# Kernel tuning notes

Hardware: AMD Instinct MI355X
Metric: run time of the kernel (lower is better)

Reference implementation:

```python
import jax, jax.numpy as jnp
import numpy as np

N_LAYERS = 5
EMB = 300
DK = 256
N_NODES = 50000
N_EDGES = 200000
B = 1000
NPER = N_NODES // B  # 50 nodes per graph (uniform -> to_dense_batch is a reshape)
PAD = 16
NUM_ATOM = 119


def setup_inputs() -> dict:
    key = jax.random.key(0)
    ks = jax.random.split(key, 24)
    f = lambda k, s: jax.random.normal(k, s, dtype=jnp.float32)
    return dict(
        x_type=jax.random.randint(ks[0], (N_NODES,), 0, NUM_ATOM, dtype=jnp.int32),
        x_feat=f(ks[1], (N_NODES, PAD)),
        edge_index=jax.random.randint(ks[2], (2, N_EDGES), 0, N_NODES, dtype=jnp.int32),
        edge_attr=jax.random.uniform(ks[3], (N_EDGES, 2), dtype=jnp.float32),
        metal_type=jax.random.randint(ks[4], (B,), 0, NUM_ATOM, dtype=jnp.int32),
        metal_feat=f(ks[5], (B, 17)),
        x_emb=f(ks[6], (NUM_ATOM, EMB)) * 0.05,
        x_weight=f(ks[7], (PAD, EMB)) * 0.05,
        ew1=f(ks[8], (N_LAYERS, 2, EMB)) * 0.05,
        mlp_w=f(ks[9], (N_LAYERS, EMB, EMB)) * 0.05,
        mlp_b=jnp.zeros((N_LAYERS, EMB), jnp.float32),
        bn_g=jnp.ones((N_LAYERS, EMB), jnp.float32),
        bn_b=jnp.zeros((N_LAYERS, EMB), jnp.float32),
        bn_rm=f(ks[10], (N_LAYERS, EMB)) * 0.1,
        bn_rv=jax.random.uniform(ks[11], (N_LAYERS, EMB), dtype=jnp.float32) + 0.5,
        me1_w=f(ks[12], (EMB, 17)) * 0.05,
        me1_b=jnp.zeros((EMB,), jnp.float32),
        me2=f(ks[13], (NUM_ATOM, EMB)) * 0.05,
        wq=f(ks[14], (DK, EMB)) * 0.05,
        wk=f(ks[15], (DK, EMB)) * 0.05,
        wv=f(ks[16], (DK, EMB)) * 0.05,
        ml_w=f(ks[17], (DK, EMB)) * 0.05,
        ml_b=jnp.zeros((DK,), jnp.float32),
        lg_w=f(ks[18], (DK, EMB)) * 0.05,
        lg_b=jnp.zeros((DK,), jnp.float32),
        ph1_w=f(ks[19], (2 * DK, DK)) * 0.05,
        ph1_b=jnp.zeros((2 * DK,), jnp.float32),
        ph2_w=f(ks[20], (1, 2 * DK)) * 0.05,
        ph2_b=jnp.zeros((1,), jnp.float32),
    )


def reference(x_type, x_feat, edge_index, edge_attr, metal_type, metal_feat,
              x_emb, x_weight, ew1, mlp_w, mlp_b, bn_g, bn_b, bn_rm, bn_rv,
              me1_w, me1_b, me2, wq, wk, wv, ml_w, ml_b, lg_w, lg_b,
              ph1_w, ph1_b, ph2_w, ph2_b):
    N = x_feat.shape[0]
    Bn = metal_feat.shape[0]
    # --- node init: atom-type embedding + feature projection ---
    h = x_emb[x_type] + x_feat @ x_weight                       # [N, 300]
    # --- metal feature: Linear(17->300) + Embedding(119,300) ---
    mf = (metal_feat @ me1_w.T + me1_b + me2[metal_type])[:, None, :]  # [B, 1, 300]
    # --- add self loops once (same every layer) ---
    loops = jnp.arange(N, dtype=edge_index.dtype)
    row = jnp.concatenate([edge_index[0], loops])               # [E+N] source
    col = jnp.concatenate([edge_index[1], loops])               # [E+N] target
    sl_attr = jnp.zeros((N, 2), edge_attr.dtype).at[:, 1].set(4.0)
    ea_full = jnp.concatenate([edge_attr, sl_attr], axis=0)     # [E+N, 2]
    eps = 1e-5
    for l in range(N_LAYERS):
        edge_fea = ea_full @ ew1[l]                             # [E+N, 300]
        # message: MLP(x_j + edge_attr), gather -> GEMM -> scatter-add
        msg = jax.nn.relu((h[row] + edge_fea) @ mlp_w[l].T + mlp_b[l])
        h = jax.ops.segment_sum(msg, col, num_segments=N)       # aggr='add'
        # BatchNorm1d (eval: running stats)
        h = (h - bn_rm[l]) * jax.lax.rsqrt(bn_rv[l] + eps) * bn_g[l] + bn_b[l]
        if l < N_LAYERS - 1:
            h = jax.nn.relu(h)  # dropout(p=0) is identity
    # --- CoordiNet, apool='none': dense batch (uniform graphs -> reshape) ---
    dense = h.reshape(Bn, -1, EMB)                              # [B, NPER, 300]
    Q = mf @ wq.T                                               # [B, 1, 256]
    K = dense @ wk.T                                            # [B, NPER, 256]
    V = dense @ wv.T
    scores = jnp.einsum('bqd,bkd->bqk', Q, K) / jnp.sqrt(jnp.asarray(DK, h.dtype))
    attention = jax.nn.softmax(scores, axis=-1) @ V             # [B, 1, 256]
    metal2 = jax.nn.relu(mf @ ml_w.T + ml_b)
    graph_fea = dense.mean(axis=1, keepdims=True)               # global_mean_pool
    lig = jax.nn.relu(graph_fea @ lg_w.T + lg_b)
    feature = jax.nn.relu(attention) + metal2 + lig             # [B, 1, 256]
    # --- pre_head: Linear -> Softplus -> Linear ---
    out = jax.nn.softplus(feature @ ph1_w.T + ph1_b) @ ph2_w.T + ph2_b  # [B, 1, 1]
    return out
```

## Files before the change

### kernel.cpp

```cpp
#include <hip/hip_runtime.h>
#include <hip/hip_bf16.h>
#include <math.h>

#define NNODES  50000
#define NEDGES  200000
#define NTOT    250000
#define EMB     300
#define LDK     320
#define MPAD    50048
#define NLAYERS 5
#define NSCAN   49
#define NPW     4

struct EdgeRec { int r; float c0, c1; };

typedef __attribute__((ext_vector_type(8))) short short8;
typedef __attribute__((ext_vector_type(4))) short short4v;
typedef __attribute__((ext_vector_type(4))) float floatx4;

__device__ inline void gll16(const void* g, void* s) {
    __builtin_amdgcn_global_load_lds((const __attribute__((address_space(1))) unsigned*)g,
                                     (__attribute__((address_space(3))) unsigned*)s, 16, 0, 0);
}

__global__ void k_trall(const float* __restrict__ wv, const float* __restrict__ lg_w,
                        const float* __restrict__ ph1_w, const float* __restrict__ me1_w,
                        float* __restrict__ wvT, float* __restrict__ lgwT,
                        float* __restrict__ ph1wT, float* __restrict__ me1wT) {
    int idx = blockIdx.x * 256 + threadIdx.x;
    if (idx < 76800) { int r = idx / 300, c = idx % 300; wvT[c * 256 + r] = wv[idx]; return; }
    idx -= 76800;
    if (idx < 76800) { int r = idx / 300, c = idx % 300; lgwT[c * 256 + r] = lg_w[idx]; return; }
    idx -= 76800;
    if (idx < 131072) { int r = idx / 256, c = idx % 256; ph1wT[c * 512 + r] = ph1_w[idx]; return; }
    idx -= 131072;
    if (idx < 5100) { int r = idx / 17, c = idx % 17; me1wT[c * 300 + r] = me1_w[idx]; }
}

__global__ void k_cvt(const float* __restrict__ w, __hip_bfloat16* __restrict__ wb) {
    int idx = blockIdx.x * 256 + threadIdx.x;
    if (idx >= 5 * 320 * 320) return;
    int l = idx / 102400, r = idx % 102400, n = r / 320, k = r % 320;
    float v = (n < 300 && k < 300) ? w[l * 90000 + n * 300 + k] : 0.f;
    wb[idx] = __float2bfloat16(v);
}

__global__ void k_cvt2(const float* __restrict__ wq, const float* __restrict__ ml_w,
                       const float* __restrict__ wk,
                       __hip_bfloat16* __restrict__ wcat, __hip_bfloat16* __restrict__ wkTb) {
    int idx = blockIdx.x * 256 + threadIdx.x;
    if (idx < 512 * 320) {
        int r = idx / 320, k = idx % 320;
        float v = 0.f;
        if (k < 300) v = (r < 256) ? wq[r * 300 + k] : ml_w[(r - 256) * 300 + k];
        wcat[idx] = __float2bfloat16(v);
        return;
    }
    idx -= 512 * 320;
    if (idx < 320 * 256) {
        int c = idx / 256, j = idx % 256;
        float v = (c < 300) ? wk[j * 300 + c] : 0.f;
        wkTb[idx] = __float2bfloat16(v);
    }
}

__global__ __launch_bounds__(256) void k_mf(const int* __restrict__ mt, const float* __restrict__ mfeat,
                                            const float* __restrict__ me1wT, const float* __restrict__ me1b,
                                            const float* __restrict__ me2,
                                            __hip_bfloat16* __restrict__ mfb) {
    int idx = blockIdx.x * 256 + threadIdx.x;
    if (idx >= 1000 * 300) return;
    int g = idx / 300, c = idx % 300;
    float v = me1b[c] + me2[(size_t)mt[g] * 300 + c];
    #pragma unroll
    for (int k = 0; k < 17; ++k) v += mfeat[g * 17 + k] * me1wT[k * 300 + c];
    mfb[(size_t)g * 320 + c] = __float2bfloat16(v);
}

__global__ __launch_bounds__(256) void k_mm(const __hip_bfloat16* __restrict__ A, int lda,
                                            const __hip_bfloat16* __restrict__ B, int ldb,
                                            int K, int mode,
                                            const float* __restrict__ mlb,
                                            __hip_bfloat16* __restrict__ qb,
                                            float* __restrict__ metal2,
                                            float* __restrict__ qkout) {
    __shared__ __hip_bfloat16 As[128 * 32];
    __shared__ __hip_bfloat16 Bs[64 * 32];
    int tid = threadIdx.x, lane = tid & 63, w = tid >> 6;
    int row0 = blockIdx.x * 128, col0 = blockIdx.y * 64;

    floatx4 acc[2][4];
    #pragma unroll
    for (int i = 0; i < 2; ++i)
        #pragma unroll
        for (int j = 0; j < 4; ++j) acc[i][j] = (floatx4){0.f, 0.f, 0.f, 0.f};

    const __hip_bfloat16* ga0 = A + (size_t)(row0 + w * 32 + (lane >> 2)) * lda + (lane & 3) * 8;
    const __hip_bfloat16* ga1 = ga0 + (size_t)16 * lda;
    const __hip_bfloat16* gb  = B + (size_t)(col0 + w * 16 + (lane >> 2)) * ldb + (lane & 3) * 8;
    __hip_bfloat16* sa0 = &As[(w * 32) * 32];
    __hip_bfloat16* sa1 = &As[(w * 32 + 16) * 32];
    __hip_bfloat16* sb  = &Bs[(w * 16) * 32];

    int m15 = lane & 15, kof = (lane >> 4) * 8;

    for (int k0 = 0; k0 < K; k0 += 32) {
        __syncthreads();
        gll16(ga0 + k0, sa0);
        gll16(ga1 + k0, sa1);
        gll16(gb  + k0, sb);
        __syncthreads();

        short8 a[2], b[4];
        a[0] = *(const short8*)&As[(w * 32 +      m15) * 32 + kof];
        a[1] = *(const short8*)&As[(w * 32 + 16 + m15) * 32 + kof];
        #pragma unroll
        for (int nt = 0; nt < 4; ++nt)
            b[nt] = *(const short8*)&Bs[(nt * 16 + m15) * 32 + kof];

        #pragma unroll
        for (int mt = 0; mt < 2; ++mt)
            #pragma unroll
            for (int nt = 0; nt < 4; ++nt)
                acc[mt][nt] = __builtin_amdgcn_mfma_f32_16x16x32_bf16(a[mt], b[nt], acc[mt][nt], 0, 0, 0);
    }

    int rbase = row0 + w * 32 + (lane >> 4) * 4;
    #pragma unroll
    for (int mt = 0; mt < 2; ++mt)
        #pragma unroll
        for (int i = 0; i < 4; ++i) {
            int gr = rbase + mt * 16 + i;
            #pragma unroll
            for (int nt = 0; nt < 4; ++nt) {
                int gc = col0 + nt * 16 + m15;
                float v = acc[mt][nt][i];
                if (mode == 0) {
                    if (gc < 256) qb[(size_t)gr * 256 + gc] = __float2bfloat16(v);
                    else if (gr < 1000) metal2[(size_t)gr * 256 + (gc - 256)] = fmaxf(v + mlb[gc - 256], 0.f);
                } else {
                    if (gc < 300 && gr < 1000) qkout[(size_t)gr * 320 + gc] = v;
                }
            }
        }
}

__global__ __launch_bounds__(256) void k_init(const int* __restrict__ xt,
                                              const float* __restrict__ xf,
                                              const float* __restrict__ xemb,
                                              const float* __restrict__ xw,
                                              __hip_bfloat16* __restrict__ h) {
    int gid = blockIdx.x * 256 + threadIdx.x;
    if (gid >= NNODES * 38) return;
    int n = gid / 38, c = (gid % 38) * 8;
    bool full = (c <= 292);
    const float* er = xemb + (size_t)xt[n] * 300 + c;
    float v[8];
    float4 e0 = *(const float4*)er;
    v[0] = e0.x; v[1] = e0.y; v[2] = e0.z; v[3] = e0.w;
    if (full) { float4 e1 = *(const float4*)(er + 4); v[4] = e1.x; v[5] = e1.y; v[6] = e1.z; v[7] = e1.w; }
    else      { v[4] = v[5] = v[6] = v[7] = 0.f; }
    float fs[16];
    const float4* xf4 = (const float4*)(xf + n * 16);
    #pragma unroll
    for (int q = 0; q < 4; ++q) {
        float4 t = xf4[q];
        fs[4 * q] = t.x; fs[4 * q + 1] = t.y; fs[4 * q + 2] = t.z; fs[4 * q + 3] = t.w;
    }
    #pragma unroll
    for (int k = 0; k < 16; ++k) {
        const float* wr = xw + k * 300 + c;
        float4 w0 = *(const float4*)wr;
        v[0] += fs[k] * w0.x; v[1] += fs[k] * w0.y; v[2] += fs[k] * w0.z; v[3] += fs[k] * w0.w;
        if (full) {
            float4 w1 = *(const float4*)(wr + 4);
            v[4] += fs[k] * w1.x; v[5] += fs[k] * w1.y; v[6] += fs[k] * w1.z; v[7] += fs[k] * w1.w;
        }
    }
    alignas(16) __hip_bfloat16 ob[8];
    #pragma unroll
    for (int i = 0; i < 8; ++i) ob[i] = __float2bfloat16(v[i]);
    __hip_bfloat16* hp = h + (size_t)n * LDK + c;
    if (full) *(short8*)hp  = *(const short8*)ob;
    else      *(short4v*)hp = *(const short4v*)ob;
}

__global__ void k_count(const int* __restrict__ ei, int* __restrict__ cnt) {
    int e = blockIdx.x * blockDim.x + threadIdx.x;
    if (e >= NTOT) return;
    int c = (e < NEDGES) ? ei[NEDGES + e] : (e - NEDGES);
    atomicAdd(&cnt[c], 1);
}

__global__ __launch_bounds__(1024) void k_scan1(const int* __restrict__ cnt, int* __restrict__ off,
                                                int* __restrict__ bsum) {
    int tid = threadIdx.x;
    int gid = blockIdx.x * 1024 + tid;
    int lane = tid & 63, wv = tid >> 6;
    int v = (gid < NNODES) ? cnt[gid] : 0;
    int x = v;
    #pragma unroll
    for (int s = 1; s < 64; s <<= 1) {
        int t = __shfl_up(x, s, 64);
        if (lane >= s) x += t;
    }
    __shared__ int wsum[16];
    if (lane == 63) wsum[wv] = x;
    __syncthreads();
    if (wv == 0) {
        int w = (lane < 16) ? wsum[lane] : 0;
        #pragma unroll
        for (int s = 1; s < 16; s <<= 1) {
            int t = __shfl_up(w, s, 64);
            if (lane >= s) w += t;
        }
        if (lane < 16) wsum[lane] = w;
    }
    __syncthreads();
    int base = (wv > 0) ? wsum[wv - 1] : 0;
    int incl = x + base;
    if (gid < NNODES) off[gid] = incl - v;
    if (tid == 1023) bsum[blockIdx.x] = incl;
}

__global__ __launch_bounds__(64) void k_scan2(int* __restrict__ bsum) {
    int lane = threadIdx.x;
    int v = (lane < NSCAN) ? bsum[lane] : 0;
    int x = v;
    #pragma unroll
    for (int s = 1; s < 64; s <<= 1) {
        int t = __shfl_up(x, s, 64);
        if (lane >= s) x += t;
    }
    if (lane < NSCAN) bsum[lane] = x - v;
}

__global__ __launch_bounds__(1024) void k_scan3(int* __restrict__ off, const int* __restrict__ bsum) {
    int gid = blockIdx.x * 1024 + threadIdx.x;
    if (gid < NNODES) off[gid] += bsum[blockIdx.x];
    if (gid == 0) off[NNODES] = NTOT;
}

__global__ void k_fill(const int* __restrict__ ei, const float* __restrict__ ea,
                       const int* __restrict__ off, int* __restrict__ cur,
                       EdgeRec* __restrict__ pack) {
    int e = blockIdx.x * blockDim.x + threadIdx.x;
    if (e >= NTOT) return;
    int r, c; float c0, c1;
    if (e < NEDGES) { r = ei[e]; c = ei[NEDGES + e]; c0 = ea[2 * e]; c1 = ea[2 * e + 1]; }
    else            { r = c = e - NEDGES; c0 = 0.f; c1 = 4.f; }
    int p = atomicAdd(&cur[c], 1);
    EdgeRec rec; rec.r = r; rec.c0 = c0; rec.c1 = c1;
    pack[off[c] + p] = rec;
}

__global__ __launch_bounds__(64) void k_prep(const float* __restrict__ mlp_w, const float* __restrict__ ew1,
                                             const float* __restrict__ mlp_b, const float* __restrict__ bn_g,
                                             const float* __restrict__ bn_b, const float* __restrict__ bn_rm,
                                             const float* __restrict__ bn_rv, float* __restrict__ prm) {
    int j = blockIdx.x, l = blockIdx.y;
    int lane = threadIdx.x;
    const float* W  = mlp_w + (size_t)l * 90000 + (size_t)j * 300;
    const float* ew = ew1 + l * 600;
    float a0 = 0.f, a1 = 0.f;
    #pragma unroll
    for (int i = 0; i < 5; ++i) {
        int k = lane + i * 64;
        if (k < 300) {
            float w = W[k];
            a0 += w * ew[k];
            a1 += w * ew[300 + k];
        }
    }
    #pragma unroll
    for (int s = 32; s > 0; s >>= 1) { a0 += __shfl_xor(a0, s, 64); a1 += __shfl_xor(a1, s, 64); }
    if (lane == 0) {
        float* p = prm + l * 1520;
        p[j] = a0;
        p[304 + j] = a1;
        p[608 + j] = mlp_b[l * 300 + j];
        float sc = bn_g[l * 300 + j] * rsqrtf(bn_rv[l * 300 + j] + 1e-5f);
        p[912 + j] = sc;
        p[1216 + j] = bn_b[l * 300 + j] - bn_rm[l * 300 + j] * sc;
    }
}

__global__ __launch_bounds__(256) void k_gemm(const __hip_bfloat16* __restrict__ A,
                                              const __hip_bfloat16* __restrict__ B,
                                              __hip_bfloat16* __restrict__ C) {
    int b = blockIdx.x;
    int rowblk = (b >> 4) * 8 + (b & 7);
    if (rowblk >= 391) return;
    int row0 = rowblk * 128;
    int col0 = ((b >> 3) & 1) * 160;

    __shared__ __hip_bfloat16 As[128 * 32];
    __shared__ __hip_bfloat16 Bs[160 * 32];
    int tid = threadIdx.x;
    int lane = tid & 63, w = tid >> 6;

    floatx4 acc[2][10];
    #pragma unroll
    for (int i = 0; i < 2; ++i)
        #pragma unroll
        for (int j = 0; j < 10; ++j) acc[i][j] = (floatx4){0.f, 0.f, 0.f, 0.f};

    const __hip_bfloat16* ga0 = A + (size_t)(row0 + w * 32 + (lane >> 2)) * LDK + (lane & 3) * 8;
    const __hip_bfloat16* ga1 = ga0 + (size_t)16 * LDK;
    __hip_bfloat16* sa0 = &As[(w * 32) * 32];
    __hip_bfloat16* sa1 = &As[(w * 32 + 16) * 32];
    int brow0 = (w < 2) ? w * 48 : 96 + (w - 2) * 32;
    int nb = (w < 2) ? 3 : 2;
    const __hip_bfloat16* gb = B + (size_t)(col0 + brow0 + (lane >> 2)) * LDK + (lane & 3) * 8;
    __hip_bfloat16* sb = &Bs[brow0 * 32];

    int m15 = lane & 15, kof = (lane >> 4) * 8;

    for (int k0 = 0; k0 < LDK; k0 += 32) {
        __syncthreads();
        gll16(ga0 + k0, sa0);
        gll16(ga1 + k0, sa1);
        for (int i = 0; i < nb; ++i)
            gll16(gb + (size_t)i * 16 * LDK + k0, sb + i * 16 * 32);
        __syncthreads();

        short8 a[2], bb[10];
        a[0] = *(const short8*)&As[(w * 32 +      m15) * 32 + kof];
        a[1] = *(const short8*)&As[(w * 32 + 16 + m15) * 32 + kof];
        #pragma unroll
        for (int nt = 0; nt < 10; ++nt)
            bb[nt] = *(const short8*)&Bs[(nt * 16 + m15) * 32 + kof];

        #pragma unroll
        for (int mt = 0; mt < 2; ++mt)
            #pragma unroll
            for (int nt = 0; nt < 10; ++nt)
                acc[mt][nt] = __builtin_amdgcn_mfma_f32_16x16x32_bf16(a[mt], bb[nt], acc[mt][nt], 0, 0, 0);
    }

    int rbase = row0 + w * 32 + (lane >> 4) * 4;
    #pragma unroll
    for (int mt = 0; mt < 2; ++mt)
        #pragma unroll
        for (int i = 0; i < 4; ++i) {
            long gr = rbase + mt * 16 + i;
            #pragma unroll
            for (int nt = 0; nt < 10; ++nt)
                C[gr * LDK + col0 + nt * 16 + m15] = __float2bfloat16(acc[mt][nt][i]);
        }
}

__global__ __launch_bounds__(256) void k_aggr(const __hip_bfloat16* __restrict__ mh,
                                              const EdgeRec* __restrict__ pack,
                                              const int* __restrict__ off, const float* __restrict__ prm,
                                              __hip_bfloat16* __restrict__ h, int do_relu) {
    int wave = threadIdx.x >> 6;
    int lane = threadIdx.x & 63;
    int n0 = (blockIdx.x * 4 + wave) * NPW;
    if (n0 >= NNODES) return;

    float u0[3][2], u1[3][2], bv[3][2], sc[3][2], sh[3][2];
    #pragma unroll
    for (int i = 0; i < 3; ++i) {
        int j = 2 * lane + 128 * i;
        #pragma unroll
        for (int t = 0; t < 2; ++t) {
            bool ok = (j + t) < 300;
            u0[i][t] = ok ? prm[j + t]        : 0.f;
            u1[i][t] = ok ? prm[304 + j + t]  : 0.f;
            bv[i][t] = ok ? prm[608 + j + t]  : 0.f;
            sc[i][t] = ok ? prm[912 + j + t]  : 0.f;
            sh[i][t] = ok ? prm[1216 + j + t] : 0.f;
        }
    }

    int nend = (n0 + NPW < NNODES) ? n0 + NPW : NNODES;
    for (int n = n0; n < nend; ++n) {
        float acc[3][2];
        #pragma unroll
        for (int i = 0; i < 3; ++i) { acc[i][0] = 0.f; acc[i][1] = 0.f; }
        int p0 = off[n], p1 = off[n + 1];
        int p = p0;
        for (; p + 1 < p1; p += 2) {
            EdgeRec e0 = pack[p], e1 = pack[p + 1];
            const __hip_bfloat16* b0 = mh + (size_t)e0.r * LDK;
            const __hip_bfloat16* b1 = mh + (size_t)e1.r * LDK;
            __hip_bfloat162 hv0[3], hv1[3];
            #pragma unroll
            for (int i = 0; i < 3; ++i) {
                int j = 2 * lane + 128 * i;
                if (j < 300) {
                    hv0[i] = *(const __hip_bfloat162*)&b0[j];
                    hv1[i] = *(const __hip_bfloat162*)&b1[j];
                }
            }
            #pragma unroll
            for (int i = 0; i < 3; ++i) {
                int j = 2 * lane + 128 * i;
                if (j < 300) {
                    acc[i][0] += fmaxf(__bfloat162float(hv0[i].x) + e0.c0 * u0[i][0] + e0.c1 * u1[i][0] + bv[i][0], 0.f);
                    acc[i][1] += fmaxf(__bfloat162float(hv0[i].y) + e0.c0 * u0[i][1] + e0.c1 * u1[i][1] + bv[i][1], 0.f);
                    acc[i][0] += fmaxf(__bfloat162float(hv1[i].x) + e1.c0 * u0[i][0] + e1.c1 * u1[i][0] + bv[i][0], 0.f);
                    acc[i][1] += fmaxf(__bfloat162float(hv1[i].y) + e1.c0 * u0[i][1] + e1.c1 * u1[i][1] + bv[i][1], 0.f);
                }
            }
        }
        if (p < p1) {
            EdgeRec e0 = pack[p];
            const __hip_bfloat16* b0 = mh + (size_t)e0.r * LDK;
            #pragma unroll
            for (int i = 0; i < 3; ++i) {
                int j = 2 * lane + 128 * i;
                if (j < 300) {
                    __hip_bfloat162 hv = *(const __hip_bfloat162*)&b0[j];
                    acc[i][0] += fmaxf(__bfloat162float(hv.x) + e0.c0 * u0[i][0] + e0.c1 * u1[i][0] + bv[i][0], 0.f);
                    acc[i][1] += fmaxf(__bfloat162float(hv.y) + e0.c0 * u0[i][1] + e0.c1 * u1[i][1] + bv[i][1], 0.f);
                }
            }
        }
        #pragma unroll
        for (int i = 0; i < 3; ++i) {
            int j = 2 * lane + 128 * i;
            if (j < 300) {
                float v0 = acc[i][0] * sc[i][0] + sh[i][0];
                float v1 = acc[i][1] * sc[i][1] + sh[i][1];
                if (do_relu) { v0 = fmaxf(v0, 0.f); v1 = fmaxf(v1, 0.f); }
                __hip_bfloat162 o;
                o.x = __float2bfloat16(v0);
                o.y = __float2bfloat16(v1);
                *(__hip_bfloat162*)&h[(size_t)n * LDK + j] = o;
            }
        }
    }
}

__global__ __launch_bounds__(320) void k_pool(const __hip_bfloat16* __restrict__ h, const float* __restrict__ qk,
                                              float* __restrict__ wpool, float* __restrict__ mean) {
    int b = blockIdx.x;
    int tid = threadIdx.x;
    int wave = tid >> 6, lane = tid & 63;
    __shared__ float qk_s[300];
    __shared__ float sc[50];
    __shared__ __hip_bfloat16 hs[50][304];
    if (tid < 300) qk_s[tid] = qk[(size_t)b * 320 + tid];
    __syncthreads();
    for (int k = wave; k < 50; k += 5) {
        const __hip_bfloat16* hp = h + (long)(b * 50 + k) * LDK;
        float partial = 0.f;
        #pragma unroll
        for (int i = 0; i < 5; ++i) {
            int j = lane + i * 64;
            if (j < 300) {
                __hip_bfloat16 hv = hp[j];
                hs[k][j] = hv;
                partial += __bfloat162float(hv) * qk_s[j];
            }
        }
        #pragma unroll
        for (int s = 32; s > 0; s >>= 1) partial += __shfl_xor(partial, s, 64);
        if (lane == 0) sc[k] = partial * (1.f / 16.f);
    }
    __syncthreads();
    if (tid == 0) {
        float mx = sc[0];
        for (int k = 1; k < 50; ++k) mx = fmaxf(mx, sc[k]);
        float s = 0.f;
        for (int k = 0; k < 50; ++k) { float e = __expf(sc[k] - mx); sc[k] = e; s += e; }
        float inv = 1.f / s;
        for (int k = 0; k < 50; ++k) sc[k] *= inv;
    }
    __syncthreads();
    if (tid < 300) {
        float aw = 0.f, am = 0.f;
        for (int k = 0; k < 50; ++k) {
            float v = __bfloat162float(hs[k][tid]);
            aw += sc[k] * v;
            am += v;
        }
        wpool[b * 300 + tid] = aw;
        mean[b * 300 + tid]  = am * (1.f / 50.f);
    }
}

__global__ __launch_bounds__(512) void k_head(const float* __restrict__ wpool, const float* __restrict__ mean,
                                              const float* __restrict__ metal2,
                                              const float* __restrict__ wvT, const float* __restrict__ lgwT,
                                              const float* __restrict__ lgb,
                                              const float* __restrict__ ph1wT, const float* __restrict__ ph1b,
                                              const float* __restrict__ ph2w, const float* __restrict__ ph2b,
                                              float* __restrict__ out) {
    int b = blockIdx.x;
    int tid = threadIdx.x;
    __shared__ float wp_s[300], mn_s[300], f_s[256], red[512];
    if (tid < 300) { wp_s[tid] = wpool[b * 300 + tid]; mn_s[tid] = mean[b * 300 + tid]; }
    __syncthreads();
    if (tid < 256) {
        float att = 0.f, lg = 0.f;
        #pragma unroll 4
        for (int k = 0; k < 300; ++k) {
            att += wp_s[k] * wvT[k * 256 + tid];
            lg  += mn_s[k] * lgwT[k * 256 + tid];
        }
        lg = fmaxf(lg + lgb[tid], 0.f);
        f_s[tid] = fmaxf(att, 0.f) + metal2[b * 256 + tid] + lg;
    }
    __syncthreads();
    float a = ph1b[tid];
    #pragma unroll 8
    for (int k = 0; k < 256; ++k) a += f_s[k] * ph1wT[k * 512 + tid];
    float sp = fmaxf(a, 0.f) + log1pf(__expf(-fabsf(a)));
    red[tid] = sp * ph2w[tid];
    __syncthreads();
    for (int s = 256; s > 0; s >>= 1) {
        if (tid < s) red[tid] += red[tid + s];
        __syncthreads();
    }
    if (tid == 0) out[b] = red[0] + ph2b[0];
}

extern "C" void kernel_launch(void* const* d_in, const int* in_sizes, int n_in,
                              void* d_out, int out_size, void* d_ws, size_t ws_size,
                              hipStream_t stream) {
    const int*   x_type   = (const int*)d_in[0];
    const float* x_feat   = (const float*)d_in[1];
    const int*   eindex   = (const int*)d_in[2];
    const float* eattr    = (const float*)d_in[3];
    const int*   mtype    = (const int*)d_in[4];
    const float* mfeat    = (const float*)d_in[5];
    const float* x_emb    = (const float*)d_in[6];
    const float* x_weight = (const float*)d_in[7];
    const float* ew1      = (const float*)d_in[8];
    const float* mlp_w    = (const float*)d_in[9];
    const float* mlp_b    = (const float*)d_in[10];
    const float* bn_g     = (const float*)d_in[11];
    const float* bn_b     = (const float*)d_in[12];
    const float* bn_rm    = (const float*)d_in[13];
    const float* bn_rv    = (const float*)d_in[14];
    const float* me1_w    = (const float*)d_in[15];
    const float* me1_b    = (const float*)d_in[16];
    const float* me2      = (const float*)d_in[17];
    const float* wq       = (const float*)d_in[18];
    const float* wk       = (const float*)d_in[19];
    const float* wv       = (const float*)d_in[20];
    const float* ml_w     = (const float*)d_in[21];
    const float* ml_b     = (const float*)d_in[22];
    const float* lg_w     = (const float*)d_in[23];
    const float* lg_b     = (const float*)d_in[24];
    const float* ph1_w    = (const float*)d_in[25];
    const float* ph1_b    = (const float*)d_in[26];
    const float* ph2_w    = (const float*)d_in[27];
    const float* ph2_b    = (const float*)d_in[28];

    char* ws = (char*)d_ws;
    size_t o = 0;
    auto alloc = [&](size_t bytes) -> void* {
        void* p = ws + o;
        o += (bytes + 255) & ~(size_t)255;
        return p;
    };
    __hip_bfloat16* h    = (__hip_bfloat16*)alloc((size_t)MPAD * LDK * 2);
    __hip_bfloat16* mh   = (__hip_bfloat16*)alloc((size_t)MPAD * LDK * 2);
    __hip_bfloat16* wb   = (__hip_bfloat16*)alloc((size_t)5 * 320 * 320 * 2);
    int*     cnt    = (int*)alloc((size_t)NNODES * 4);
    int*     offs   = (int*)alloc((size_t)(NNODES + 1) * 4);
    int*     cur    = (int*)alloc((size_t)NNODES * 4);
    int*     bsum   = (int*)alloc((size_t)64 * 4);
    EdgeRec* pack   = (EdgeRec*)alloc((size_t)NTOT * sizeof(EdgeRec));
    float*   prm    = (float*)alloc((size_t)NLAYERS * 1520 * 4);
    float*   metal2 = (float*)alloc((size_t)1000 * 256 * 4);
    float*   qk     = (float*)alloc((size_t)1024 * 320 * 4);
    float*   wpool  = (float*)alloc((size_t)1000 * 300 * 4);
    float*   meanp  = (float*)alloc((size_t)1000 * 300 * 4);
    float*   wvT    = (float*)alloc((size_t)300 * 256 * 4);
    float*   lgwT   = (float*)alloc((size_t)300 * 256 * 4);
    float*   ph1wT  = (float*)alloc((size_t)256 * 512 * 4);
    float*   me1wT  = (float*)alloc((size_t)17 * 300 * 4);
    __hip_bfloat16* mfb  = (__hip_bfloat16*)alloc((size_t)1024 * 320 * 2);
    __hip_bfloat16* wcat = (__hip_bfloat16*)alloc((size_t)512 * 320 * 2);
    __hip_bfloat16* wkTb = (__hip_bfloat16*)alloc((size_t)320 * 256 * 2);
    __hip_bfloat16* qb   = (__hip_bfloat16*)alloc((size_t)1024 * 256 * 2);
    (void)ws_size; (void)in_sizes; (void)n_in; (void)out_size;

    hipMemsetAsync(cnt, 0, (size_t)NNODES * 4, stream);
    hipMemsetAsync(cur, 0, (size_t)NNODES * 4, stream);
    hipMemsetAsync(mfb, 0, (size_t)1024 * 320 * 2, stream);

    k_cvt<<<(5 * 320 * 320 + 255) / 256, 256, 0, stream>>>(mlp_w, wb);
    k_cvt2<<<(512 * 320 + 320 * 256 + 255) / 256, 256, 0, stream>>>(wq, ml_w, wk, wcat, wkTb);
    k_trall<<<(289772 + 255) / 256, 256, 0, stream>>>(wv, lg_w, ph1_w, me1_w, wvT, lgwT, ph1wT, me1wT);
    k_init<<<(NNODES * 38 + 255) / 256, 256, 0, stream>>>(x_type, x_feat, x_emb, x_weight, h);
    k_count<<<(NTOT + 255) / 256, 256, 0, stream>>>(eindex, cnt);
    k_scan1<<<NSCAN, 1024, 0, stream>>>(cnt, offs, bsum);
    k_scan2<<<1, 64, 0, stream>>>(bsum);
    k_scan3<<<NSCAN, 1024, 0, stream>>>(offs, bsum);
    k_fill<<<(NTOT + 255) / 256, 256, 0, stream>>>(eindex, eattr, offs, cur, pack);
    {
        dim3 gp(300, NLAYERS);
        k_prep<<<gp, 64, 0, stream>>>(mlp_w, ew1, mlp_b, bn_g, bn_b, bn_rm, bn_rv, prm);
    }
    k_mf<<<(1000 * 300 + 255) / 256, 256, 0, stream>>>(mtype, mfeat, me1wT, me1_b, me2, mfb);
    {
        dim3 g1(8, 8);
        k_mm<<<g1, 256, 0, stream>>>(mfb, 320, wcat, 320, 320, 0, ml_b, qb, metal2, qk);
        dim3 g2(8, 5);
        k_mm<<<g2, 256, 0, stream>>>(qb, 256, wkTb, 256, 256, 1, ml_b, qb, metal2, qk);
    }

    for (int l = 0; l < NLAYERS; ++l) {
        k_gemm<<<784, 256, 0, stream>>>(h, wb + (size_t)l * 102400, mh);
        int aggr_grid = (NNODES + 4 * NPW - 1) / (4 * NPW);
        k_aggr<<<aggr_grid, 256, 0, stream>>>(mh, pack, offs, prm + (size_t)l * 1520, h,
                                              (l < NLAYERS - 1) ? 1 : 0);
    }

    k_pool<<<1000, 320, 0, stream>>>(h, qk, wpool, meanp);
    k_head<<<1000, 512, 0, stream>>>(wpool, meanp, metal2, wvT, lgwT, lg_b,
                                     ph1wT, ph1_b, ph2_w, ph2_b, (float*)d_out);
}
```

Measured before the change: 612.4 us.

## Move node init and prediction head onto bf16 MFMA GEMMs

The node-initialisation feature projection is recast as a small bf16 MFMA GEMM (features padded to K=32) with the atom-embedding add fused into the epilogue. The per-graph scalar head kernel, which reread the transposed fp32 weights in every block, is split into tiled bf16 MFMA GEMMs for the attention-value, ligand and first pre-head projections, plus small elementwise combine and softplus/reduce kernels. The aim is to replace scalar FMA loops and repeated weight traffic with matrix-core work. In exchange it adds extra conversion passes and intermediate buffers, lowers the head to bf16 precision, and reads unwritten pad columns of the pooled buffers, which are only safe if that workspace holds no NaN or Inf.

```diff
diff --git a/kernel.cpp b/kernel.cpp
--- a/kernel.cpp
+++ b/kernel.cpp
@@ -15,26 +15,11 @@
 struct EdgeRec { int r; float c0, c1; };
 
 typedef __attribute__((ext_vector_type(8))) short short8;
-typedef __attribute__((ext_vector_type(4))) short short4v;
 typedef __attribute__((ext_vector_type(4))) float floatx4;
 
 __device__ inline void gll16(const void* g, void* s) {
     __builtin_amdgcn_global_load_lds((const __attribute__((address_space(1))) unsigned*)g,
                                      (__attribute__((address_space(3))) unsigned*)s, 16, 0, 0);
-}
-
-__global__ void k_trall(const float* __restrict__ wv, const float* __restrict__ lg_w,
-                        const float* __restrict__ ph1_w, const float* __restrict__ me1_w,
-                        float* __restrict__ wvT, float* __restrict__ lgwT,
-                        float* __restrict__ ph1wT, float* __restrict__ me1wT) {
-    int idx = blockIdx.x * 256 + threadIdx.x;
-    if (idx < 76800) { int r = idx / 300, c = idx % 300; wvT[c * 256 + r] = wv[idx]; return; }
-    idx -= 76800;
-    if (idx < 76800) { int r = idx / 300, c = idx % 300; lgwT[c * 256 + r] = lg_w[idx]; return; }
-    idx -= 76800;
-    if (idx < 131072) { int r = idx / 256, c = idx % 256; ph1wT[c * 512 + r] = ph1_w[idx]; return; }
-    idx -= 131072;
-    if (idx < 5100) { int r = idx / 17, c = idx % 17; me1wT[c * 300 + r] = me1_w[idx]; }
 }
 
 __global__ void k_cvt(const float* __restrict__ w, __hip_bfloat16* __restrict__ wb) {
@@ -62,6 +47,36 @@
         float v = (c < 300) ? wk[j * 300 + c] : 0.f;
         wkTb[idx] = __float2bfloat16(v);
     }
+}
+
+__global__ void k_cvt3(const float* __restrict__ xf, const float* __restrict__ xw,
+                       const float* __restrict__ wv, const float* __restrict__ lg_w,
+                       const float* __restrict__ ph1_w, const float* __restrict__ me1_w,
+                       __hip_bfloat16* __restrict__ xfb, __hip_bfloat16* __restrict__ xwTb,
+                       __hip_bfloat16* __restrict__ wvB, __hip_bfloat16* __restrict__ lgwB,
+                       __hip_bfloat16* __restrict__ ph1wb, float* __restrict__ me1wT) {
+    int idx = blockIdx.x * 256 + threadIdx.x;
+    if (idx < 1601536) {
+        int n = idx >> 5, k = idx & 31;
+        xfb[idx] = __float2bfloat16((n < 50000 && k < 16) ? xf[n * 16 + k] : 0.f);
+        return;
+    }
+    idx -= 1601536;
+    if (idx < 10240) {
+        int n = idx >> 5, k = idx & 31;
+        xwTb[idx] = __float2bfloat16((n < 300 && k < 16) ? xw[k * 300 + n] : 0.f);
+        return;
+    }
+    idx -= 10240;
+    if (idx < 81920) { int r = idx / 320, k = idx % 320;
+        wvB[idx] = __float2bfloat16((k < 300) ? wv[r * 300 + k] : 0.f); return; }
+    idx -= 81920;
+    if (idx < 81920) { int r = idx / 320, k = idx % 320;
+        lgwB[idx] = __float2bfloat16((k < 300) ? lg_w[r * 300 + k] : 0.f); return; }
+    idx -= 81920;
+    if (idx < 131072) { ph1wb[idx] = __float2bfloat16(ph1_w[idx]); return; }
+    idx -= 131072;
+    if (idx < 5100) { int r = idx / 17, c = idx % 17; me1wT[c * 300 + r] = me1_w[idx]; }
 }
 
 __global__ __launch_bounds__(256) void k_mf(const int* __restrict__ mt, const float* __restrict__ mfeat,
@@ -145,44 +160,130 @@
         }
 }
 
-__global__ __launch_bounds__(256) void k_init(const int* __restrict__ xt,
-                                              const float* __restrict__ xf,
-                                              const float* __restrict__ xemb,
-                                              const float* __restrict__ xw,
-                                              __hip_bfloat16* __restrict__ h) {
-    int gid = blockIdx.x * 256 + threadIdx.x;
-    if (gid >= NNODES * 38) return;
-    int n = gid / 38, c = (gid % 38) * 8;
-    bool full = (c <= 292);
-    const float* er = xemb + (size_t)xt[n] * 300 + c;
-    float v[8];
-    float4 e0 = *(const float4*)er;
-    v[0] = e0.x; v[1] = e0.y; v[2] = e0.z; v[3] = e0.w;
-    if (full) { float4 e1 = *(const float4*)(er + 4); v[4] = e1.x; v[5] = e1.y; v[6] = e1.z; v[7] = e1.w; }
-    else      { v[4] = v[5] = v[6] = v[7] = 0.f; }
-    float fs[16];
-    const float4* xf4 = (const float4*)(xf + n * 16);
-    #pragma unroll
-    for (int q = 0; q < 4; ++q) {
-        float4 t = xf4[q];
-        fs[4 * q] = t.x; fs[4 * q + 1] = t.y; fs[4 * q + 2] = t.z; fs[4 * q + 3] = t.w;
-    }
-    #pragma unroll
-    for (int k = 0; k < 16; ++k) {
-        const float* wr = xw + k * 300 + c;
-        float4 w0 = *(const float4*)wr;
-        v[0] += fs[k] * w0.x; v[1] += fs[k] * w0.y; v[2] += fs[k] * w0.z; v[3] += fs[k] * w0.w;
-        if (full) {
-            float4 w1 = *(const float4*)(wr + 4);
-            v[4] += fs[k] * w1.x; v[5] += fs[k] * w1.y; v[6] += fs[k] * w1.z; v[7] += fs[k] * w1.w;
-        }
-    }
-    alignas(16) __hip_bfloat16 ob[8];
-    #pragma unroll
-    for (int i = 0; i < 8; ++i) ob[i] = __float2bfloat16(v[i]);
-    __hip_bfloat16* hp = h + (size_t)n * LDK + c;
-    if (full) *(short8*)hp  = *(const short8*)ob;
-    else      *(short4v*)hp = *(const short4v*)ob;
+__global__ __launch_bounds__(256) void k_mm2(const __hip_bfloat16* __restrict__ A, int lda,
+                                             const __hip_bfloat16* __restrict__ B, int ldb,
+                                             int K, float* __restrict__ C, int ldc) {
+    __shared__ __hip_bfloat16 As[128 * 32];
+    __shared__ __hip_bfloat16 Bs[64 * 32];
+    int tid = threadIdx.x, lane = tid & 63, w = tid >> 6;
+    int row0 = blockIdx.x * 128, col0 = blockIdx.y * 64;
+
+    floatx4 acc[2][4];
+    #pragma unroll
+    for (int i = 0; i < 2; ++i)
+        #pragma unroll
+        for (int j = 0; j < 4; ++j) acc[i][j] = (floatx4){0.f, 0.f, 0.f, 0.f};
+
+    const __hip_bfloat16* ga0 = A + (size_t)(row0 + w * 32 + (lane >> 2)) * lda + (lane & 3) * 8;
+    const __hip_bfloat16* ga1 = ga0 + (size_t)16 * lda;
+    const __hip_bfloat16* gb  = B + (size_t)(col0 + w * 16 + (lane >> 2)) * ldb + (lane & 3) * 8;
+    __hip_bfloat16* sa0 = &As[(w * 32) * 32];
+    __hip_bfloat16* sa1 = &As[(w * 32 + 16) * 32];
+    __hip_bfloat16* sb  = &Bs[(w * 16) * 32];
+
+    int m15 = lane & 15, kof = (lane >> 4) * 8;
+
+    for (int k0 = 0; k0 < K; k0 += 32) {
+        __syncthreads();
+        gll16(ga0 + k0, sa0);
+        gll16(ga1 + k0, sa1);
+        gll16(gb  + k0, sb);
+        __syncthreads();
+
+        short8 a[2], b[4];
+        a[0] = *(const short8*)&As[(w * 32 +      m15) * 32 + kof];
+        a[1] = *(const short8*)&As[(w * 32 + 16 + m15) * 32 + kof];
+        #pragma unroll
+        for (int nt = 0; nt < 4; ++nt)
+            b[nt] = *(const short8*)&Bs[(nt * 16 + m15) * 32 + kof];
+
+        #pragma unroll
+        for (int mt = 0; mt < 2; ++mt)
+            #pragma unroll
+            for (int nt = 0; nt < 4; ++nt)
+                acc[mt][nt] = __builtin_amdgcn_mfma_f32_16x16x32_bf16(a[mt], b[nt], acc[mt][nt], 0, 0, 0);
+    }
+
+    int rbase = row0 + w * 32 + (lane >> 4) * 4;
+    #pragma unroll
+    for (int mt = 0; mt < 2; ++mt)
+        #pragma unroll
+        for (int i = 0; i < 4; ++i) {
+            int gr = rbase + mt * 16 + i;
+            #pragma unroll
+            for (int nt = 0; nt < 4; ++nt)
+                C[(size_t)gr * ldc + col0 + nt * 16 + m15] = acc[mt][nt][i];
+        }
+}
+
+__global__ __launch_bounds__(256) void k_initg(const __hip_bfloat16* __restrict__ A,
+                                               const __hip_bfloat16* __restrict__ B,
+                                               const int* __restrict__ xt,
+                                               const float* __restrict__ xemb,
+                                               __hip_bfloat16* __restrict__ h) {
+    int b = blockIdx.x;
+    int rowblk = (b >> 4) * 8 + (b & 7);
+    if (rowblk >= 391) return;
+    int row0 = rowblk * 128;
+    int col0 = ((b >> 3) & 1) * 160;
+
+    __shared__ __hip_bfloat16 As[128 * 32];
+    __shared__ __hip_bfloat16 Bs[160 * 32];
+    int tid = threadIdx.x;
+    int lane = tid & 63, w = tid >> 6;
+
+    floatx4 acc[2][10];
+    #pragma unroll
+    for (int i = 0; i < 2; ++i)
+        #pragma unroll
+        for (int j = 0; j < 10; ++j) acc[i][j] = (floatx4){0.f, 0.f, 0.f, 0.f};
+
+    const __hip_bfloat16* ga0 = A + (size_t)(row0 + w * 32 + (lane >> 2)) * 32 + (lane & 3) * 8;
+    const __hip_bfloat16* ga1 = ga0 + (size_t)16 * 32;
+    __hip_bfloat16* sa0 = &As[(w * 32) * 32];
+    __hip_bfloat16* sa1 = &As[(w * 32 + 16) * 32];
+    int brow0 = (w < 2) ? w * 48 : 96 + (w - 2) * 32;
+    int nb = (w < 2) ? 3 : 2;
+    const __hip_bfloat16* gb = B + (size_t)(col0 + brow0 + (lane >> 2)) * 32 + (lane & 3) * 8;
+    __hip_bfloat16* sb = &Bs[brow0 * 32];
+
+    int m15 = lane & 15, kof = (lane >> 4) * 8;
+
+    gll16(ga0, sa0);
+    gll16(ga1, sa1);
+    for (int i = 0; i < nb; ++i)
+        gll16(gb + (size_t)i * 16 * 32, sb + i * 16 * 32);
+    __syncthreads();
+
+    short8 a[2], bb[10];
+    a[0] = *(const short8*)&As[(w * 32 +      m15) * 32 + kof];
+    a[1] = *(const short8*)&As[(w * 32 + 16 + m15) * 32 + kof];
+    #pragma unroll
+    for (int nt = 0; nt < 10; ++nt)
+        bb[nt] = *(const short8*)&Bs[(nt * 16 + m15) * 32 + kof];
+
+    #pragma unroll
+    for (int mt = 0; mt < 2; ++mt)
+        #pragma unroll
+        for (int nt = 0; nt < 10; ++nt)
+            acc[mt][nt] = __builtin_amdgcn_mfma_f32_16x16x32_bf16(a[mt], bb[nt], acc[mt][nt], 0, 0, 0);
+
+    int rbase = row0 + w * 32 + (lane >> 4) * 4;
+    #pragma unroll
+    for (int mt = 0; mt < 2; ++mt)
+        #pragma unroll
+        for (int i = 0; i < 4; ++i) {
+            int gr = rbase + mt * 16 + i;
+            if (gr < NNODES) {
+                const float* er = xemb + (size_t)xt[gr] * 300;
+                #pragma unroll
+                for (int nt = 0; nt < 10; ++nt) {
+                    int gc = col0 + nt * 16 + m15;
+                    if (gc < 300)
+                        h[(size_t)gr * LDK + gc] = __float2bfloat16(acc[mt][nt][i] + er[gc]);
+                }
+            }
+        }
 }
 
 __global__ void k_count(const int* __restrict__ ei, int* __restrict__ cnt) {
@@ -435,7 +536,7 @@
 }
 
 __global__ __launch_bounds__(320) void k_pool(const __hip_bfloat16* __restrict__ h, const float* __restrict__ qk,
-                                              float* __restrict__ wpool, float* __restrict__ mean) {
+                                              __hip_bfloat16* __restrict__ wpb, __hip_bfloat16* __restrict__ mnb) {
     int b = blockIdx.x;
     int tid = threadIdx.x;
     int wave = tid >> 6, lane = tid & 63;
@@ -477,45 +578,40 @@
             aw += sc[k] * v;
             am += v;
         }
-        wpool[b * 300 + tid] = aw;
-        mean[b * 300 + tid]  = am * (1.f / 50.f);
-    }
-}
-
-__global__ __launch_bounds__(512) void k_head(const float* __restrict__ wpool, const float* __restrict__ mean,
-                                              const float* __restrict__ metal2,
-                                              const float* __restrict__ wvT, const float* __restrict__ lgwT,
-                                              const float* __restrict__ lgb,
-                                              const float* __restrict__ ph1wT, const float* __restrict__ ph1b,
-                                              const float* __restrict__ ph2w, const float* __restrict__ ph2b,
-                                              float* __restrict__ out) {
-    int b = blockIdx.x;
-    int tid = threadIdx.x;
-    __shared__ float wp_s[300], mn_s[300], f_s[256], red[512];
-    if (tid < 300) { wp_s[tid] = wpool[b * 300 + tid]; mn_s[tid] = mean[b * 300 + tid]; }
+        wpb[(size_t)b * 320 + tid] = __float2bfloat16(aw);
+        mnb[(size_t)b * 320 + tid] = __float2bfloat16(am * (1.f / 50.f));
+    }
+}
+
+__global__ void k_comb(const float* __restrict__ attb, const float* __restrict__ ligb,
+                       const float* __restrict__ metal2, const float* __restrict__ lg_bias,
+                       __hip_bfloat16* __restrict__ fb) {
+    int idx = blockIdx.x * 256 + threadIdx.x;
+    if (idx >= 1000 * 256) return;
+    int c = idx & 255;
+    float f = fmaxf(attb[idx], 0.f) + metal2[idx] + fmaxf(ligb[idx] + lg_bias[c], 0.f);
+    fb[idx] = __float2bfloat16(f);
+}
+
+__global__ __launch_bounds__(512) void k_out(const float* __restrict__ a2, const float* __restrict__ ph1b,
+                                             const float* __restrict__ ph2w, const float* __restrict__ ph2b,
+                                             float* __restrict__ out) {
+    int b = blockIdx.x, t = threadIdx.x;
+    int lane = t & 63, wv = t >> 6;
+    float a = a2[(size_t)b * 512 + t] + ph1b[t];
+    float sp = fmaxf(a, 0.f) + log1pf(__expf(-fabsf(a)));
+    float r = sp * ph2w[t];
+    #pragma unroll
+    for (int s = 32; s > 0; s >>= 1) r += __shfl_xor(r, s, 64);
+    __shared__ float red[8];
+    if (lane == 0) red[wv] = r;
     __syncthreads();
-    if (tid < 256) {
-        float att = 0.f, lg = 0.f;
-        #pragma unroll 4
-        for (int k = 0; k < 300; ++k) {
-            att += wp_s[k] * wvT[k * 256 + tid];
-            lg  += mn_s[k] * lgwT[k * 256 + tid];
-        }
-        lg = fmaxf(lg + lgb[tid], 0.f);
-        f_s[tid] = fmaxf(att, 0.f) + metal2[b * 256 + tid] + lg;
-    }
-    __syncthreads();
-    float a = ph1b[tid];
-    #pragma unroll 8
-    for (int k = 0; k < 256; ++k) a += f_s[k] * ph1wT[k * 512 + tid];
-    float sp = fmaxf(a, 0.f) + log1pf(__expf(-fabsf(a)));
-    red[tid] = sp * ph2w[tid];
-    __syncthreads();
-    for (int s = 256; s > 0; s >>= 1) {
-        if (tid < s) red[tid] += red[tid + s];
-        __syncthreads();
-    }
-    if (tid == 0) out[b] = red[0] + ph2b[0];
+    if (t == 0) {
+        float s = 0.f;
+        #pragma unroll
+        for (int i = 0; i < 8; ++i) s += red[i];
+        out[b] = s + ph2b[0];
+    }
 }
 
 extern "C" void kernel_launch(void* const* d_in, const int* in_sizes, int n_in,
@@ -569,16 +665,22 @@
     float*   prm    = (float*)alloc((size_t)NLAYERS * 1520 * 4);
     float*   metal2 = (float*)alloc((size_t)1000 * 256 * 4);
     float*   qk     = (float*)alloc((size_t)1024 * 320 * 4);
-    float*   wpool  = (float*)alloc((size_t)1000 * 300 * 4);
-    float*   meanp  = (float*)alloc((size_t)1000 * 300 * 4);
-    float*   wvT    = (float*)alloc((size_t)300 * 256 * 4);
-    float*   lgwT   = (float*)alloc((size_t)300 * 256 * 4);
-    float*   ph1wT  = (float*)alloc((size_t)256 * 512 * 4);
     float*   me1wT  = (float*)alloc((size_t)17 * 300 * 4);
     __hip_bfloat16* mfb  = (__hip_bfloat16*)alloc((size_t)1024 * 320 * 2);
     __hip_bfloat16* wcat = (__hip_bfloat16*)alloc((size_t)512 * 320 * 2);
     __hip_bfloat16* wkTb = (__hip_bfloat16*)alloc((size_t)320 * 256 * 2);
     __hip_bfloat16* qb   = (__hip_bfloat16*)alloc((size_t)1024 * 256 * 2);
+    __hip_bfloat16* xfb  = (__hip_bfloat16*)alloc((size_t)MPAD * 32 * 2);
+    __hip_bfloat16* xwTb = (__hip_bfloat16*)alloc((size_t)320 * 32 * 2);
+    __hip_bfloat16* wvB  = (__hip_bfloat16*)alloc((size_t)256 * 320 * 2);
+    __hip_bfloat16* lgwB = (__hip_bfloat16*)alloc((size_t)256 * 320 * 2);
+    __hip_bfloat16* ph1wb= (__hip_bfloat16*)alloc((size_t)512 * 256 * 2);
+    __hip_bfloat16* wpb  = (__hip_bfloat16*)alloc((size_t)1024 * 320 * 2);
+    __hip_bfloat16* mnb  = (__hip_bfloat16*)alloc((size_t)1024 * 320 * 2);
+    float*   attb   = (float*)alloc((size_t)1024 * 256 * 4);
+    float*   ligb   = (float*)alloc((size_t)1024 * 256 * 4);
+    __hip_bfloat16* fb = (__hip_bfloat16*)alloc((size_t)1024 * 256 * 2);
+    float*   a2     = (float*)alloc((size_t)1024 * 512 * 4);
     (void)ws_size; (void)in_sizes; (void)n_in; (void)out_size;
 
     hipMemsetAsync(cnt, 0, (size_t)NNODES * 4, stream);
@@ -587,8 +689,9 @@
 
     k_cvt<<<(5 * 320 * 320 + 255) / 256, 256, 0, stream>>>(mlp_w, wb);
     k_cvt2<<<(512 * 320 + 320 * 256 + 255) / 256, 256, 0, stream>>>(wq, ml_w, wk, wcat, wkTb);
-    k_trall<<<(289772 + 255) / 256, 256, 0, stream>>>(wv, lg_w, ph1_w, me1_w, wvT, lgwT, ph1wT, me1wT);
-    k_init<<<(NNODES * 38 + 255) / 256, 256, 0, stream>>>(x_type, x_feat, x_emb, x_weight, h);
+    k_cvt3<<<(1911788 + 255) / 256, 256, 0, stream>>>(x_feat, x_weight, wv, lg_w, ph1_w, me1_w,
+                                                      xfb, xwTb, wvB, lgwB, ph1wb, me1wT);
+    k_initg<<<784, 256, 0, stream>>>(xfb, xwTb, x_type, x_emb, h);
     k_count<<<(NTOT + 255) / 256, 256, 0, stream>>>(eindex, cnt);
     k_scan1<<<NSCAN, 1024, 0, stream>>>(cnt, offs, bsum);
     k_scan2<<<1, 64, 0, stream>>>(bsum);
@@ -613,7 +716,14 @@
                                               (l < NLAYERS - 1) ? 1 : 0);
     }
 
-    k_pool<<<1000, 320, 0, stream>>>(h, qk, wpool, meanp);
-    k_head<<<1000, 512, 0, stream>>>(wpool, meanp, metal2, wvT, lgwT, lg_b,
-                                     ph1wT, ph1_b, ph2_w, ph2_b, (float*)d_out);
-}
+    k_pool<<<1000, 320, 0, stream>>>(h, qk, wpb, mnb);
+    {
+        dim3 ga(8, 4);
+        k_mm2<<<ga, 256, 0, stream>>>(wpb, 320, wvB, 320, 320, attb, 256);
+        k_mm2<<<ga, 256, 0, stream>>>(mnb, 320, lgwB, 320, 320, ligb, 256);
+        k_comb<<<(1000 * 256 + 255) / 256, 256, 0, stream>>>(attb, ligb, metal2, lg_b, fb);
+        dim3 gph(8, 8);
+        k_mm2<<<gph, 256, 0, stream>>>(fb, 256, ph1wb, 256, 256, a2, 512);
+        k_out<<<1000, 512, 0, stream>>>(a2, ph1_b, ph2_w, ph2_b, (float*)d_out);
+    }
+}
```

After: 566.8 us. 7.4% less time.
